# Kernel tuning notes

Hardware: AMD Instinct MI355X
Metric: run time of the kernel (lower is better)

## Reference

```python
import jax, jax.numpy as jnp
import numpy as np

NUM_CLASSES = 10
MAX_V = 81  # max_width * max_height = 9*9


def _ln(x, w, eps=1e-5):
    # torch LayerNorm with bias=False (weight only)
    m = jnp.mean(x, axis=-1, keepdims=True)
    v = jnp.var(x, axis=-1, keepdims=True)
    return (x - m) / jnp.sqrt(v + eps) * w


def _mha(q_in, k_in, v_in, in_proj, out_proj, nhead):
    # torch nn.MultiheadAttention, bias=False
    d = q_in.shape[-1]
    Wq, Wk, Wv = in_proj[:d], in_proj[d:2 * d], in_proj[2 * d:]
    q = q_in @ Wq.T
    k = k_in @ Wk.T
    v = v_in @ Wv.T
    B, Lq, _ = q.shape
    Lk = k.shape[1]
    hd = d // nhead
    q = q.reshape(B, Lq, nhead, hd)
    k = k.reshape(B, Lk, nhead, hd)
    v = v.reshape(B, Lk, nhead, hd)
    scores = jnp.einsum('bqhd,bkhd->bhqk', q, k) / jnp.sqrt(jnp.asarray(hd, q.dtype))
    attn = jax.nn.softmax(scores, axis=-1)
    o = jnp.einsum('bhqk,bkhd->bqhd', attn, v).reshape(B, Lq, d)
    return o @ out_proj.T


def setup_inputs() -> dict:
    key = jax.random.key(0)
    ks = jax.random.split(key, 16)
    N, C, H, W = 16, NUM_CLASSES, 30, 30
    d = C + 1  # 11
    V = 32

    def rn(k, shape, s=0.2):
        return (jax.random.normal(k, shape) * s).astype(jnp.float32)

    return {
        'x': jax.random.normal(ks[0], (N, C, H, W), dtype=jnp.float32),
        'V_feature': rn(ks[1], (C, V), 1.0),
        'enc_in_proj': rn(ks[2], (3 * d, d)),
        'enc_out_proj': rn(ks[3], (d, d)),
        'enc_lin1': rn(ks[4], (1, d)),
        'enc_lin2': rn(ks[5], (d, 1)),
        'enc_ln1': jnp.ones((d,), jnp.float32),
        'enc_ln2': jnp.ones((d,), jnp.float32),
        'ffV_w': rn(ks[6], (V, MAX_V)),
        'dec_sa_in': rn(ks[7], (3 * V, V)),
        'dec_sa_out': rn(ks[8], (V, V)),
        'dec_ca_in': rn(ks[9], (3 * V, V)),
        'dec_ca_out': rn(ks[10], (V, V)),
        'dec_lin1': rn(ks[11], (1, V)),
        'dec_lin2': rn(ks[12], (V, 1)),
        'dec_ln1': jnp.ones((V,), jnp.float32),
        'dec_ln2': jnp.ones((V,), jnp.float32),
        'dec_ln3': jnp.ones((V,), jnp.float32),
        'W_d0': rn(ks[13], (8, V)),
        'W_d1': rn(ks[14], (1, 8)),
    }


def reference(x, V_feature, enc_in_proj, enc_out_proj, enc_lin1, enc_lin2,
              enc_ln1, enc_ln2, ffV_w, dec_sa_in, dec_sa_out, dec_ca_in,
              dec_ca_out, dec_lin1, dec_lin2, dec_ln1, dec_ln2, dec_ln3,
              W_d0, W_d1):
    N, C, H, W = x.shape
    # PixelVectorExtractor: pad(0) + all-ones channel padded with 1, 3x3 unfold
    xp = jnp.pad(x, ((0, 0), (0, 0), (1, 1), (1, 1)))
    ones = jnp.ones((N, 1, H + 2, W + 2), x.dtype)
    xc = jnp.concatenate([xp, ones], axis=1)  # [N, C+1, H+2, W+2]
    # row-major 3x3 patch order matches torch unfold(0,3,1).unfold(1,3,1)
    patches = jnp.stack([xc[:, :, di:di + H, dj:dj + W]
                         for di in range(3) for dj in range(3)], axis=-1)
    feat = patches.transpose(0, 2, 3, 1, 4).reshape(N * H * W, C + 1, 9)
    feat = jnp.pad(feat, ((0, 0), (0, 0), (0, MAX_V - 9)))  # [B, C+1, 81]

    # TransformerEncoder (1 layer, post-norm, nhead=1, relu FF, no dropout)
    f = feat.transpose(0, 2, 1)  # [B, 81, C+1]
    f = _ln(f + _mha(f, f, f, enc_in_proj, enc_out_proj, 1), enc_ln1)
    f = _ln(f + jax.nn.relu(f @ enc_lin1.T) @ enc_lin2.T, enc_ln2)
    f = f.transpose(0, 2, 1)  # [B, C+1, 81]

    mem = f @ ffV_w.T  # ff_V: Linear(81 -> 32, no bias) -> [B, C+1, 32]
    B, _, V = mem.shape

    # TransformerDecoder (1 layer, post-norm, nhead=32 so head_dim=1)
    y = jnp.broadcast_to(V_feature, (B, C, V))
    y = _ln(y + _mha(y, y, y, dec_sa_in, dec_sa_out, V), dec_ln1)
    y = _ln(y + _mha(y, mem, mem, dec_ca_in, dec_ca_out, V), dec_ln2)
    y = _ln(y + jax.nn.relu(y @ dec_lin1.T) @ dec_lin2.T, dec_ln3)

    # decode MLP: 32 -> 8 -> 1
    y = jax.nn.relu(y @ W_d0.T) @ W_d1.T  # [B, C, 1]
    return y.reshape(N, H, W, C).transpose(0, 3, 1, 2)
```

## Files before the change

kernel.cpp:

```cpp
#include <hip/hip_runtime.h>
#include <math.h>


#define LOG2E 1.4426950408889634f

#define F9o   0
#define Go    112
#define VOTo  224
#define SCo   368
#define ZRo   512
#define FETo  640
#define OCo   0
#define SLICE 784

#define SWZ_ADD(v, pat) ((v) + __int_as_float(__builtin_amdgcn_ds_swizzle(__float_as_int(v), (pat))))

__device__ __forceinline__ void wsync() {
  asm volatile("s_waitcnt lgkmcnt(0)" ::: "memory");
}

__global__ __launch_bounds__(256) void precompute_kernel(
    const float* __restrict__ Vf,
    const float* __restrict__ enc_in,
    const float* __restrict__ enc_outw,
    const float* __restrict__ ffV_w,
    const float* __restrict__ dec_sa_in,
    const float* __restrict__ dec_sa_out,
    const float* __restrict__ dec_ln1,
    const float* __restrict__ dec_ca_in,
    const float* __restrict__ dec_ln2v, const float* __restrict__ dec_lin1,
    const float* __restrict__ dec_lin2, const float* __restrict__ dec_ln3v,
    const float* __restrict__ W_d0,
    float* __restrict__ M_enc, float* __restrict__ WVO,
    float* __restrict__ G_k, float* __restrict__ G_v,
    float* __restrict__ y1, float* __restrict__ qca, float* __restrict__ hc)
{
  const int tid = threadIdx.x;

  if (blockIdx.x == 0) {
    const float rs11 = 0.3015113445777636f;
    for (int idx = tid; idx < 121; idx += 256) {
      int c = idx / 11, cp = idx - c * 11;
      float sm = 0.f, sv = 0.f;
      for (int i = 0; i < 11; ++i) {
        sm += enc_in[i * 11 + c] * enc_in[(11 + i) * 11 + cp];
        sv += enc_outw[c * 11 + i] * enc_in[(22 + i) * 11 + cp];
      }
      M_enc[idx] = sm * rs11 * LOG2E;
      WVO[idx] = sv;
    }

    __shared__ float Fsh[320];
    for (int idx = tid; idx < 288; idx += 256) {
      int t = idx >> 5, j = idx & 31;
      Fsh[idx] = ffV_w[j * 81 + t];
    }
    if (tid < 32) {
      float s = 0.f;
      for (int t = 9; t < 81; ++t) s += ffV_w[tid * 81 + t];
      Fsh[288 + tid] = s;
    }
    __syncthreads();

    for (int idx = tid; idx < 640; idx += 256) {
      int which = idx >= 320;
      int r = idx - 320 * which;
      int t = r >> 5, h = r & 31;
      const float* w = dec_ca_in + ((which ? 64 : 32) + h) * 32;
      float s = 0.f;
      for (int j = 0; j < 32; ++j) s += Fsh[t * 32 + j] * w[j];
      (which ? G_v : G_k)[r] = s;
    }

    if (tid < 8) {
      float u = 0.f, t2 = 0.f, v = 0.f;
      for (int c = 0; c < 32; ++c) {
        float w0 = W_d0[tid * 32 + c] * dec_ln3v[c];
        u += dec_ln2v[c] * w0;
        t2 += dec_lin2[c] * w0;
        v += w0;
      }
      hc[tid] = u; hc[8 + tid] = t2; hc[16 + tid] = v;
    } else if (tid == 8) {
      float a = 0, b = 0, c2 = 0, d = 0, e = 0, f = 0;
      for (int c = 0; c < 32; ++c) {
        float w2 = dec_ln2v[c], l2 = dec_lin2[c];
        a += w2; b += w2 * dec_lin1[c]; c2 += w2 * w2;
        d += w2 * l2; e += l2; f += l2 * l2;
      }
      hc[24] = a; hc[25] = b; hc[26] = c2; hc[27] = d; hc[28] = e; hc[29] = f;
    }
  } else {
    __shared__ float qsa[320], ksa[320], vsa[320], osa[320], zb[320];
    __shared__ float mu[16], rstd[16];

    for (int idx = tid; idx < 960; idx += 256) {
      int m = idx / 320, r = idx - m * 320;
      int t = r >> 5, h = r & 31;
      const float* w = dec_sa_in + (m * 32 + h) * 32;
      const float* yr = Vf + t * 32;
      float s = 0.f;
#pragma unroll
      for (int j = 0; j < 32; ++j) s += yr[j] * w[j];
      (m == 0 ? qsa : m == 1 ? ksa : vsa)[r] = s;
    }
    __syncthreads();

    for (int idx = tid; idx < 320; idx += 256) {
      int h = idx & 31;
      float q = qsa[idx];
      float sc[10];
      float mx = -1e30f;
#pragma unroll
      for (int s = 0; s < 10; ++s) { sc[s] = q * ksa[s * 32 + h]; mx = fmaxf(mx, sc[s]); }
      float den = 0.f, acc = 0.f;
#pragma unroll
      for (int s = 0; s < 10; ++s) {
        float e = __expf(sc[s] - mx);
        den += e;
        acc += e * vsa[s * 32 + h];
      }
      osa[idx] = acc / den;
    }
    __syncthreads();

    for (int idx = tid; idx < 320; idx += 256) {
      int t = idx >> 5, c = idx & 31;
      float s = 0.f;
#pragma unroll
      for (int h = 0; h < 32; ++h) s += osa[t * 32 + h] * dec_sa_out[c * 32 + h];
      zb[idx] = Vf[idx] + s;
    }
    __syncthreads();

    if (tid < 10) {
      float s1 = 0.f, s2 = 0.f;
      for (int c = 0; c < 32; ++c) { float z = zb[tid * 32 + c]; s1 += z; s2 += z * z; }
      float m = s1 * (1.f / 32.f);
      mu[tid] = m;
      rstd[tid] = 1.f / sqrtf(s2 * (1.f / 32.f) - m * m + 1e-5f);
    }
    __syncthreads();

    for (int idx = tid; idx < 320; idx += 256) {
      int t = idx >> 5, c = idx & 31;
      float v = (zb[idx] - mu[t]) * rstd[t] * dec_ln1[c];
      y1[idx] = v;
      zb[idx] = v;
    }
    __syncthreads();

    for (int idx = tid; idx < 320; idx += 256) {
      int t = idx >> 5, h = idx & 31;
      const float* w = dec_ca_in + h * 32;
      float s = 0.f;
#pragma unroll
      for (int j = 0; j < 32; ++j) s += zb[t * 32 + j] * w[j];
      qca[idx] = s * LOG2E;
    }
  }
}

__global__ __launch_bounds__(256) void pixel_main_kernel(
    const float* __restrict__ x,
    const float* __restrict__ M_enc, const float* __restrict__ WVO,
    const float* __restrict__ enc_lin1, const float* __restrict__ enc_lin2,
    const float* __restrict__ enc_ln1, const float* __restrict__ enc_ln2,
    const float* __restrict__ G_k, const float* __restrict__ G_v,
    const float* __restrict__ y1g, const float* __restrict__ qcag,
    const float* __restrict__ dec_ca_out,
    const float* __restrict__ dec_ln2v, const float* __restrict__ dec_lin1,
    const float* __restrict__ dec_lin2, const float* __restrict__ dec_ln3v,
    const float* __restrict__ W_d0, const float* __restrict__ W_d1,
    const float* __restrict__ hc,
    float* __restrict__ out)
{
  __shared__ __align__(16) float sh[4 * SLICE + 256];
  float* bc = sh + 4 * SLICE;
  for (int i = threadIdx.x; i < 121; i += 256) {
    bc[i] = M_enc[i];
    bc[128 + i] = WVO[i];
  }
  __syncthreads();

  const int wave = threadIdx.x >> 6;
  const int lane = threadIdx.x & 63;
  float* ls = sh + wave * SLICE;

  const int p = blockIdx.x * 4 + wave;
  const int n = p / 900;
  const int rem = p - n * 900;
  const int pi = rem / 30, pj = rem - (rem / 30) * 30;

  for (int idx = lane; idx < 99; idx += 64) {
    int t = idx / 11, c = idx - t * 11;
    float val = 1.0f;
    if (c < 10) {
      int di = t / 3, dj = t - (t / 3) * 3;
      int ii = pi + di - 1, jj = pj + dj - 1;
      val = (ii >= 0 && ii < 30 && jj >= 0 && jj < 30)
                ? x[((n * 10 + c) * 30 + ii) * 30 + jj] : 0.0f;
    }
    ls[F9o + t * 12 + c] = val;
  }
  if (lane < 12) ls[SCo + 108 + lane] = (lane < 9) ? (1.0f / 81.0f) : 0.0f;
  wsync();

  for (int idx = lane; idx < 99; idx += 64) {
    int s = idx / 11, c = idx - (idx / 11) * 11;
    const float4* fr = (const float4*)(ls + F9o + s * 12);
    float4 f0 = fr[0], f1 = fr[1], f2 = fr[2];
    float fv[11] = {f0.x, f0.y, f0.z, f0.w, f1.x, f1.y, f1.z, f1.w, f2.x, f2.y, f2.z};
    const float* Mr = bc + c * 11;
    const float* Wr = bc + 128 + c * 11;
    float ag = 0.f, av = 0.f;
#pragma unroll
    for (int cp = 0; cp < 11; ++cp) { ag += Mr[cp] * fv[cp]; av += Wr[cp] * fv[cp]; }
    ls[Go + s * 12 + c] = ag;
    ls[VOTo + c * 12 + s] = av;
  }
  wsync();

  for (int idx = lane; idx < 81; idx += 64) {
    int t = idx / 9, s = idx - (idx / 9) * 9;
    const float4* fr = (const float4*)(ls + F9o + t * 12);
    const float4* gr = (const float4*)(ls + Go + s * 12);
    float4 f0 = fr[0], f1 = fr[1], f2 = fr[2];
    float4 g0 = gr[0], g1 = gr[1], g2 = gr[2];
    float a = f0.x * g0.x + f0.y * g0.y + f0.z * g0.z + f0.w * g0.w
            + f1.x * g1.x + f1.y * g1.y + f1.z * g1.z + f1.w * g1.w
            + f2.x * g2.x + f2.y * g2.y + f2.z * g2.z;
    ls[SCo + t * 12 + s] = a;
  }
  wsync();

  if (lane < 9) {
    const float4* sr = (const float4*)(ls + SCo + lane * 12);
    float4 s0 = sr[0], s1 = sr[1];
    float sc[9] = {s0.x, s0.y, s0.z, s0.w, s1.x, s1.y, s1.z, s1.w,
                   ls[SCo + lane * 12 + 8]};
    float mx = 0.0f;
#pragma unroll
    for (int s = 0; s < 9; ++s) mx = fmaxf(mx, sc[s]);
    float den = 72.0f * exp2f(-mx);
    float e[12];
    e[9] = e[10] = e[11] = 0.f;
#pragma unroll
    for (int s = 0; s < 9; ++s) { e[s] = exp2f(sc[s] - mx); den += e[s]; }
    float4* dst = (float4*)(ls + SCo + lane * 12);
    dst[0] = make_float4(e[0], e[1], e[2], e[3]);
    dst[1] = make_float4(e[4], e[5], e[6], e[7]);
    dst[2] = make_float4(e[8], 0.f, 0.f, 0.f);
    ls[SCo + 120 + lane] = __builtin_amdgcn_rcpf(den);
  }
  wsync();

  for (int idx = lane; idx < 110; idx += 64) {
    int t = idx / 11, c = idx - (idx / 11) * 11;
    const float4* wr = (const float4*)(ls + SCo + t * 12);
    const float4* vr = (const float4*)(ls + VOTo + c * 12);
    float4 w0 = wr[0], w1 = wr[1], w2q = wr[2];
    float4 v0 = vr[0], v1 = vr[1], v2 = vr[2];
    float a = w0.x * v0.x + w0.y * v0.y + w0.z * v0.z + w0.w * v0.w
            + w1.x * v1.x + w1.y * v1.y + w1.z * v1.z + w1.w * v1.w
            + w2q.x * v2.x;
    if (t < 9) a = a * ls[SCo + 120 + t] + ls[F9o + t * 12 + c];
    ls[ZRo + t * 12 + c] = a;
  }
  wsync();

  if (lane < 10) {
    const float4* zr = (const float4*)(ls + ZRo + lane * 12);
    float4 z0 = zr[0], z1 = zr[1], z2q = zr[2];
    float row[11] = {z0.x, z0.y, z0.z, z0.w, z1.x, z1.y, z1.z, z1.w,
                     z2q.x, z2q.y, z2q.z};
    float s1 = 0.f, s2 = 0.f;
#pragma unroll
    for (int c = 0; c < 11; ++c) { s1 += row[c]; s2 += row[c] * row[c]; }
    float mu = s1 * (1.0f / 11.0f);
    float rs = __builtin_amdgcn_rsqf(s2 * (1.0f / 11.0f) - mu * mu + 1e-5f);
    float h = 0.f;
#pragma unroll
    for (int c = 0; c < 11; ++c) {
      row[c] = (row[c] - mu) * rs * enc_ln1[c];
      h += row[c] * enc_lin1[c];
    }
    h = fmaxf(h, 0.f);
    float t1 = 0.f, t2 = 0.f;
#pragma unroll
    for (int c = 0; c < 11; ++c) {
      row[c] += h * enc_lin2[c];
      t1 += row[c]; t2 += row[c] * row[c];
    }
    float mu2 = t1 * (1.0f / 11.0f);
    float rs2 = __builtin_amdgcn_rsqf(t2 * (1.0f / 11.0f) - mu2 * mu2 + 1e-5f);
#pragma unroll
    for (int c = 0; c < 11; ++c)
      ls[FETo + c * 12 + lane] = (row[c] - mu2) * rs2 * enc_ln2[c];
  }
  wsync();

  const int hh = lane & 31, grp = lane >> 5;
  float kv[11];
  {
    const float* Gb = grp ? G_v : G_k;
    float gr[10];
#pragma unroll
    for (int t = 0; t < 10; ++t) gr[t] = Gb[t * 32 + hh];
#pragma unroll
    for (int cc = 0; cc < 11; ++cc) {
      const float4* fr = (const float4*)(ls + FETo + cc * 12);
      float4 a = fr[0], b4 = fr[1], c4 = fr[2];
      float fe[10] = {a.x, a.y, a.z, a.w, b4.x, b4.y, b4.z, b4.w, c4.x, c4.y};
      float s = 0.f;
#pragma unroll
      for (int t = 0; t < 10; ++t) s += fe[t] * gr[t];
      kv[cc] = s;
    }
  }
  float kk[11], vv[11];
#pragma unroll
  for (int cc = 0; cc < 11; ++cc) {
    float o = __shfl_xor(kv[cc], 32);
    kk[cc] = grp ? o : kv[cc];
    vv[cc] = grp ? kv[cc] : o;
  }

#pragma unroll
  for (int i = 0; i < 5; ++i) {
    int t = grp * 5 + i;
    float q = qcag[t * 32 + hh];
    float sc[11];
    float mx = q * kk[0];
    sc[0] = mx;
#pragma unroll
    for (int s = 1; s < 11; ++s) { sc[s] = q * kk[s]; mx = fmaxf(mx, sc[s]); }
    float den = 0.f, acc = 0.f;
#pragma unroll
    for (int s = 0; s < 11; ++s) {
      float e = exp2f(sc[s] - mx);
      den += e;
      acc += e * vv[s];
    }
    ls[OCo + t * 32 + hh] = acc * __builtin_amdgcn_rcpf(den);
  }
  wsync();

  const int c = hh;
  float w2 = dec_ln2v[c], cl1 = dec_lin1[c], cl2 = dec_lin2[c], w3 = dec_ln3v[c];
  float cw2l1 = w2 * cl1, cw2sq = w2 * w2, cw2l2 = w2 * cl2;
  float am[8], Uu[8], Tt[8], Vv[8], W1r[8];
#pragma unroll
  for (int m = 0; m < 8; ++m) {
    am[m] = w2 * w3 * W_d0[m * 32 + c];
    Uu[m] = hc[m]; Tt[m] = hc[8 + m]; Vv[m] = hc[16 + m]; W1r[m] = W_d1[m];
  }
  const float Sw2 = hc[24], Sw2l1 = hc[25], Sw2sq = hc[26], Sw2l2 = hc[27],
              Sl2 = hc[28], Sl2sq = hc[29];
  const float4* wrow = (const float4*)(dec_ca_out + c * 32);

#pragma unroll
  for (int k = 0; k < 5; ++k) {
    const int t = 2 * k + grp;
    float z = y1g[t * 32 + c];
    const float4* orow = (const float4*)(ls + OCo + t * 32);
#pragma unroll
    for (int h4 = 0; h4 < 8; ++h4) {
      float4 o4 = orow[h4];
      float4 w4 = wrow[h4];
      z += o4.x * w4.x + o4.y * w4.y + o4.z * w4.z + o4.w * w4.w;
    }
    float b[15];
    b[0] = z; b[1] = z * z; b[2] = z * w2; b[3] = z * cw2l1;
    b[4] = z * cw2sq; b[5] = b[1] * cw2sq; b[6] = z * cw2l2;
#pragma unroll
    for (int m = 0; m < 8; ++m) b[7 + m] = z * am[m];
#pragma unroll
    for (int i_ = 0; i_ < 15; ++i_) b[i_] = SWZ_ADD(b[i_], 0x041F);
#pragma unroll
    for (int i_ = 0; i_ < 15; ++i_) b[i_] = SWZ_ADD(b[i_], 0x081F);
#pragma unroll
    for (int i_ = 0; i_ < 15; ++i_) b[i_] = SWZ_ADD(b[i_], 0x101F);
#pragma unroll
    for (int i_ = 0; i_ < 15; ++i_) b[i_] = SWZ_ADD(b[i_], 0x201F);
#pragma unroll
    for (int i_ = 0; i_ < 15; ++i_) b[i_] = SWZ_ADD(b[i_], 0x401F);

    const float inv32 = 1.0f / 32.0f;
    float mu = b[0] * inv32;
    float rs = __builtin_amdgcn_rsqf(b[1] * inv32 - mu * mu + 1e-5f);
    float d1 = rs * (b[3] - mu * Sw2l1);
    float h1 = fmaxf(d1, 0.f);
    float sz2 = rs * (b[2] - mu * Sw2);
    float sz2sq = rs * rs * (b[5] - 2.f * mu * b[4] + mu * mu * Sw2sq);
    float sz2l2 = rs * (b[6] - mu * Sw2l2);
    float sz3 = sz2 + h1 * Sl2;
    float sz3q = sz2sq + 2.f * h1 * sz2l2 + h1 * h1 * Sl2sq;
    float mu3 = sz3 * inv32;
    float rs3 = __builtin_amdgcn_rsqf(sz3q * inv32 - mu3 * mu3 + 1e-5f);
    float r = 0.f;
#pragma unroll
    for (int m = 0; m < 8; ++m) {
      float gm = rs3 * (rs * (b[7 + m] - mu * Uu[m]) + h1 * Tt[m] - mu3 * Vv[m]);
      r += fmaxf(gm, 0.f) * W1r[m];
    }
    if (c == 0) out[((n * 10 + t) * 30 + pi) * 30 + pj] = r;
  }
}

extern "C" void kernel_launch(void* const* d_in, const int* in_sizes, int n_in,
                              void* d_out, int out_size, void* d_ws, size_t ws_size,
                              hipStream_t stream) {
  (void)in_sizes; (void)n_in; (void)out_size; (void)ws_size;
  const float* x          = (const float*)d_in[0];
  const float* Vf         = (const float*)d_in[1];
  const float* enc_in     = (const float*)d_in[2];
  const float* enc_outw   = (const float*)d_in[3];
  const float* enc_lin1   = (const float*)d_in[4];
  const float* enc_lin2   = (const float*)d_in[5];
  const float* enc_ln1    = (const float*)d_in[6];
  const float* enc_ln2    = (const float*)d_in[7];
  const float* ffV_w      = (const float*)d_in[8];
  const float* dec_sa_in  = (const float*)d_in[9];
  const float* dec_sa_out = (const float*)d_in[10];
  const float* dec_ca_in  = (const float*)d_in[11];
  const float* dec_ca_out = (const float*)d_in[12];
  const float* dec_lin1   = (const float*)d_in[13];
  const float* dec_lin2   = (const float*)d_in[14];
  const float* dec_ln1    = (const float*)d_in[15];
  const float* dec_ln2    = (const float*)d_in[16];
  const float* dec_ln3    = (const float*)d_in[17];
  const float* W_d0       = (const float*)d_in[18];
  const float* W_d1       = (const float*)d_in[19];
  float* out = (float*)d_out;

  float* ws    = (float*)d_ws;
  float* M_enc = ws;
  float* WVO   = ws + 128;
  float* G_k   = ws + 256;
  float* G_v   = ws + 576;
  float* y1    = ws + 896;
  float* qca   = ws + 1216;
  float* hcw   = ws + 1536;

  hipLaunchKernelGGL(precompute_kernel, dim3(2), dim3(256), 0, stream,
                     Vf, enc_in, enc_outw, ffV_w, dec_sa_in, dec_sa_out,
                     dec_ln1, dec_ca_in, dec_ln2, dec_lin1, dec_lin2, dec_ln3,
                     W_d0, M_enc, WVO, G_k, G_v, y1, qca, hcw);

  hipLaunchKernelGGL(pixel_main_kernel, dim3(3600), dim3(256), 0, stream,
                     x, M_enc, WVO, enc_lin1, enc_lin2, enc_ln1, enc_ln2,
                     G_k, G_v, y1, qca, dec_ca_out, dec_ln2, dec_lin1,
                     dec_lin2, dec_ln3, W_d0, W_d1, hcw, out);
}
```

Baseline: 186.7 us.

## Replace algebraic moment-sum decoder tail with explicit LayerNorms and LDS MLP

The decoder tail no longer propagates 15 moment sums through swizzle reductions to fold LN2, FF, LN3 and the first MLP layer algebraically. It now computes the normalized values explicitly with two small shuffle reductions, writes the LN3 output to LDS, and does the 32->8 MLP and the final 8->1 dot as separate LDS passes. The precompute kernel is simplified to pack per-channel weights into a float4 table. This removes many cross-lane reductions but adds LDS round trips and extra wave syncs, and the MLP pass uses only part of the wave.

After: 298.1 us. 59.7% more time.

```diff
diff --git a/kernel.cpp b/kernel.cpp
--- a/kernel.cpp
+++ b/kernel.cpp
@@ -11,9 +11,8 @@
 #define ZRo   512
 #define FETo  640
 #define OCo   0
+#define ZBo   384
 #define SLICE 784
-
-#define SWZ_ADD(v, pat) ((v) + __int_as_float(__builtin_amdgcn_ds_swizzle(__float_as_int(v), (pat))))
 
 __device__ __forceinline__ void wsync() {
   asm volatile("s_waitcnt lgkmcnt(0)" ::: "memory");
@@ -30,10 +29,9 @@
     const float* __restrict__ dec_ca_in,
     const float* __restrict__ dec_ln2v, const float* __restrict__ dec_lin1,
     const float* __restrict__ dec_lin2, const float* __restrict__ dec_ln3v,
-    const float* __restrict__ W_d0,
     float* __restrict__ M_enc, float* __restrict__ WVO,
     float* __restrict__ G_k, float* __restrict__ G_v,
-    float* __restrict__ y1, float* __restrict__ qca, float* __restrict__ hc)
+    float* __restrict__ y1, float* __restrict__ qca, float* __restrict__ t4w)
 {
   const int tid = threadIdx.x;
 
@@ -72,23 +70,13 @@
       (which ? G_v : G_k)[r] = s;
     }
 
-    if (tid < 8) {
-      float u = 0.f, t2 = 0.f, v = 0.f;
-      for (int c = 0; c < 32; ++c) {
-        float w0 = W_d0[tid * 32 + c] * dec_ln3v[c];
-        u += dec_ln2v[c] * w0;
-        t2 += dec_lin2[c] * w0;
-        v += w0;
-      }
-      hc[tid] = u; hc[8 + tid] = t2; hc[16 + tid] = v;
-    } else if (tid == 8) {
-      float a = 0, b = 0, c2 = 0, d = 0, e = 0, f = 0;
-      for (int c = 0; c < 32; ++c) {
-        float w2 = dec_ln2v[c], l2 = dec_lin2[c];
-        a += w2; b += w2 * dec_lin1[c]; c2 += w2 * w2;
-        d += w2 * l2; e += l2; f += l2 * l2;
-      }
-      hc[24] = a; hc[25] = b; hc[26] = c2; hc[27] = d; hc[28] = e; hc[29] = f;
+    if (tid < 32) {
+      float w2 = dec_ln2v[tid], l1 = dec_lin1[tid];
+      ((float4*)t4w)[tid] = make_float4(w2, w2 * l1, dec_lin2[tid], dec_ln3v[tid]);
+    } else if (tid == 32) {
+      float s = 0.f;
+      for (int c = 0; c < 32; ++c) s += dec_ln2v[c] * dec_lin1[c];
+      t4w[128] = s;
     }
   } else {
     __shared__ float qsa[320], ksa[320], vsa[320], osa[320], zb[320];
@@ -169,10 +157,8 @@
     const float* __restrict__ G_k, const float* __restrict__ G_v,
     const float* __restrict__ y1g, const float* __restrict__ qcag,
     const float* __restrict__ dec_ca_out,
-    const float* __restrict__ dec_ln2v, const float* __restrict__ dec_lin1,
-    const float* __restrict__ dec_lin2, const float* __restrict__ dec_ln3v,
     const float* __restrict__ W_d0, const float* __restrict__ W_d1,
-    const float* __restrict__ hc,
+    const float* __restrict__ t4w,
     float* __restrict__ out)
 {
   __shared__ __align__(16) float sh[4 * SLICE + 256];
@@ -243,8 +229,7 @@
 #pragma unroll
     for (int s = 0; s < 9; ++s) mx = fmaxf(mx, sc[s]);
     float den = 72.0f * exp2f(-mx);
-    float e[12];
-    e[9] = e[10] = e[11] = 0.f;
+    float e[9];
 #pragma unroll
     for (int s = 0; s < 9; ++s) { e[s] = exp2f(sc[s] - mx); den += e[s]; }
     float4* dst = (float4*)(ls + SCo + lane * 12);
@@ -347,17 +332,10 @@
   wsync();
 
   const int c = hh;
-  float w2 = dec_ln2v[c], cl1 = dec_lin1[c], cl2 = dec_lin2[c], w3 = dec_ln3v[c];
-  float cw2l1 = w2 * cl1, cw2sq = w2 * w2, cw2l2 = w2 * cl2;
-  float am[8], Uu[8], Tt[8], Vv[8], W1r[8];
-#pragma unroll
-  for (int m = 0; m < 8; ++m) {
-    am[m] = w2 * w3 * W_d0[m * 32 + c];
-    Uu[m] = hc[m]; Tt[m] = hc[8 + m]; Vv[m] = hc[16 + m]; W1r[m] = W_d1[m];
-  }
-  const float Sw2 = hc[24], Sw2l1 = hc[25], Sw2sq = hc[26], Sw2l2 = hc[27],
-              Sl2 = hc[28], Sl2sq = hc[29];
+  const float4 t4 = ((const float4*)t4w)[c];
+  const float Sw2l1 = t4w[128];
   const float4* wrow = (const float4*)(dec_ca_out + c * 32);
+  const float inv32 = 1.0f / 32.0f;
 
 #pragma unroll
   for (int k = 0; k < 5; ++k) {
@@ -370,41 +348,49 @@
       float4 w4 = wrow[h4];
       z += o4.x * w4.x + o4.y * w4.y + o4.z * w4.z + o4.w * w4.w;
     }
-    float b[15];
-    b[0] = z; b[1] = z * z; b[2] = z * w2; b[3] = z * cw2l1;
-    b[4] = z * cw2sq; b[5] = b[1] * cw2sq; b[6] = z * cw2l2;
-#pragma unroll
-    for (int m = 0; m < 8; ++m) b[7 + m] = z * am[m];
-#pragma unroll
-    for (int i_ = 0; i_ < 15; ++i_) b[i_] = SWZ_ADD(b[i_], 0x041F);
-#pragma unroll
-    for (int i_ = 0; i_ < 15; ++i_) b[i_] = SWZ_ADD(b[i_], 0x081F);
-#pragma unroll
-    for (int i_ = 0; i_ < 15; ++i_) b[i_] = SWZ_ADD(b[i_], 0x101F);
-#pragma unroll
-    for (int i_ = 0; i_ < 15; ++i_) b[i_] = SWZ_ADD(b[i_], 0x201F);
-#pragma unroll
-    for (int i_ = 0; i_ < 15; ++i_) b[i_] = SWZ_ADD(b[i_], 0x401F);
-
-    const float inv32 = 1.0f / 32.0f;
-    float mu = b[0] * inv32;
-    float rs = __builtin_amdgcn_rsqf(b[1] * inv32 - mu * mu + 1e-5f);
-    float d1 = rs * (b[3] - mu * Sw2l1);
-    float h1 = fmaxf(d1, 0.f);
-    float sz2 = rs * (b[2] - mu * Sw2);
-    float sz2sq = rs * rs * (b[5] - 2.f * mu * b[4] + mu * mu * Sw2sq);
-    float sz2l2 = rs * (b[6] - mu * Sw2l2);
-    float sz3 = sz2 + h1 * Sl2;
-    float sz3q = sz2sq + 2.f * h1 * sz2l2 + h1 * h1 * Sl2sq;
-    float mu3 = sz3 * inv32;
-    float rs3 = __builtin_amdgcn_rsqf(sz3q * inv32 - mu3 * mu3 + 1e-5f);
+    float a0 = z, a1 = z * z, a2 = z * t4.y;
+#pragma unroll
+    for (int m = 16; m > 0; m >>= 1) {
+      a0 += __shfl_xor(a0, m, 32);
+      a1 += __shfl_xor(a1, m, 32);
+      a2 += __shfl_xor(a2, m, 32);
+    }
+    float mu = a0 * inv32;
+    float rs = __builtin_amdgcn_rsqf(a1 * inv32 - mu * mu + 1e-5f);
+    float h1 = fmaxf(rs * (a2 - mu * Sw2l1), 0.f);
+    float z3 = (z - mu) * rs * t4.x + h1 * t4.z;
+    float b0 = z3, b1 = z3 * z3;
+#pragma unroll
+    for (int m = 16; m > 0; m >>= 1) {
+      b0 += __shfl_xor(b0, m, 32);
+      b1 += __shfl_xor(b1, m, 32);
+    }
+    float mu3 = b0 * inv32;
+    float rs3 = __builtin_amdgcn_rsqf(b1 * inv32 - mu3 * mu3 + 1e-5f);
+    ls[ZBo + t * 32 + c] = (z3 - mu3) * rs3 * t4.w;
+  }
+  wsync();
+
+  for (int idx = lane; idx < 80; idx += 64) {
+    int t = idx >> 3, m = idx & 7;
+    const float4* arow = (const float4*)(W_d0 + m * 32);
+    const float4* zrow4 = (const float4*)(ls + ZBo + t * 32);
+    float d = 0.f;
+#pragma unroll
+    for (int q4 = 0; q4 < 8; ++q4) {
+      float4 a4 = arow[q4];
+      float4 z4 = zrow4[q4];
+      d += a4.x * z4.x + a4.y * z4.y + a4.z * z4.z + a4.w * z4.w;
+    }
+    ls[OCo + idx] = fmaxf(d, 0.f);
+  }
+  wsync();
+
+  if (lane < 10) {
     float r = 0.f;
 #pragma unroll
-    for (int m = 0; m < 8; ++m) {
-      float gm = rs3 * (rs * (b[7 + m] - mu * Uu[m]) + h1 * Tt[m] - mu3 * Vv[m]);
-      r += fmaxf(gm, 0.f) * W1r[m];
-    }
-    if (c == 0) out[((n * 10 + t) * 30 + pi) * 30 + pj] = r;
+    for (int m = 0; m < 8; ++m) r += ls[OCo + lane * 8 + m] * W_d1[m];
+    out[((n * 10 + lane) * 30 + pi) * 30 + pj] = r;
   }
 }
 
@@ -441,15 +427,14 @@
   float* G_v   = ws + 576;
   float* y1    = ws + 896;
   float* qca   = ws + 1216;
-  float* hcw   = ws + 1536;
+  float* t4w   = ws + 1536;
 
   hipLaunchKernelGGL(precompute_kernel, dim3(2), dim3(256), 0, stream,
                      Vf, enc_in, enc_outw, ffV_w, dec_sa_in, dec_sa_out,
                      dec_ln1, dec_ca_in, dec_ln2, dec_lin1, dec_lin2, dec_ln3,
-                     W_d0, M_enc, WVO, G_k, G_v, y1, qca, hcw);
+                     M_enc, WVO, G_k, G_v, y1, qca, t4w);
 
   hipLaunchKernelGGL(pixel_main_kernel, dim3(3600), dim3(256), 0, stream,
                      x, M_enc, WVO, enc_lin1, enc_lin2, enc_ln1, enc_ln2,
-                     G_k, G_v, y1, qca, dec_ca_out, dec_ln2, dec_lin1,
-                     dec_lin2, dec_ln3, W_d0, W_d1, hcw, out);
+                     G_k, G_v, y1, qca, dec_ca_out, W_d0, W_d1, t4w, out);
 }
```
